# Kernel optimization log

Measured on AMD Instinct MI355X. Metric: run time of the kernel, lower is better.

Reference implementation:

```python
import jax, jax.numpy as jnp
from jax import lax
import numpy as np

B = 32768
N_IN = 8
N_HID = 64
N_CTRL = 2
M_SCEN = (1.0, 1.2)          # scenario parameters for f/g
M_NOM = 1.0
CLF_LAM = 1.0
CBF_LAM = 1.0
P_CLF = 100.0
P_CBF = 50.0
QP_ITERS = 80                # fixed-iteration batched ADMM (OSQP-style) replacing CvxpyLayer
RHO = 1.0
SIGMA = 1e-6
INF = jnp.inf


def setup_inputs() -> dict:
    key = jax.random.key(0)
    ks = jax.random.split(key, 16)
    s = 0.3
    return {
        "x":   jax.random.normal(ks[0], (B, N_IN), jnp.float32),
        "VW1": jax.random.normal(ks[1], (N_HID, N_IN), jnp.float32) * s,
        "Vb1": jax.random.normal(ks[2], (N_HID,), jnp.float32) * s,
        "VW2": jax.random.normal(ks[3], (N_HID, N_HID), jnp.float32) * s,
        "Vb2": jax.random.normal(ks[4], (N_HID,), jnp.float32) * s,
        "HW1": jax.random.normal(ks[5], (N_HID, N_IN), jnp.float32) * s,
        "Hb1": jax.random.normal(ks[6], (N_HID,), jnp.float32) * s,
        "HW2": jax.random.normal(ks[7], (N_HID, N_HID), jnp.float32) * s,
        "Hb2": jax.random.normal(ks[8], (N_HID,), jnp.float32) * s,
        "HW3": jax.random.normal(ks[9], (N_HID, N_HID), jnp.float32) * s,
        "Hb3": jax.random.normal(ks[10], (N_HID,), jnp.float32) * s,
        "HW4": jax.random.normal(ks[11], (1, N_HID), jnp.float32) * s,
        "Hb4": jax.random.normal(ks[12], (1,), jnp.float32) * s,
        "G0":  jax.random.normal(ks[13], (N_IN, N_CTRL), jnp.float32) * s,
        "K":   jax.random.normal(ks[14], (N_IN, N_CTRL), jnp.float32) * s,
    }


def _lyapunov(x, W1, b1, W2, b2):
    t1 = jnp.tanh(x @ W1.T + b1)                                   # [B,H]
    t2 = jnp.tanh(t1 @ W2.T + b2)                                  # [B,H]
    V = 0.5 * jnp.sum(t2 * t2, axis=1)                             # [B]
    # fused diag(1-t^2) @ W chain (no diag_embed materialization)
    D1 = (1.0 - t1 ** 2)[:, :, None] * W1[None]                    # [B,H,N]
    D2 = (1.0 - t2 ** 2)[:, :, None] * jnp.einsum('hk,bkn->bhn', W2, D1)
    grad_V = jnp.einsum('bh,bhn->bn', t2, D2)                      # [B,N]
    return V, grad_V


def _barrier(x, W1, b1, W2, b2, W3, b3, W4, b4):
    t1 = jnp.tanh(x @ W1.T + b1)
    t2 = jnp.tanh(t1 @ W2.T + b2)
    t3 = jnp.tanh(t2 @ W3.T + b3)
    H = t3 @ W4.T + b4                                             # [B,1]
    D1 = (1.0 - t1 ** 2)[:, :, None] * W1[None]
    D2 = (1.0 - t2 ** 2)[:, :, None] * jnp.einsum('hk,bkn->bhn', W2, D1)
    D3 = (1.0 - t3 ** 2)[:, :, None] * jnp.einsum('hk,bkn->bhn', W3, D2)
    grad_H = jnp.einsum('oh,bhn->bn', W4, D3)                      # [B,N] (o=1)
    return H, grad_H


def _solve_qp(q, A, lo, hi):
    """Batched OSQP-style ADMM for min 0.5 z^T P z + q^T z  s.t. lo <= A z <= hi.
    P = diag([2,2,0,0,0,0]); z = [u(2), r_clf(2), s_cbf(2)]. Fixed iterations."""
    nb, mc, nz = A.shape[0], A.shape[1], A.shape[2]
    Pdiag = jnp.array([2.0, 2.0, 0.0, 0.0, 0.0, 0.0], q.dtype)
    M = RHO * jnp.einsum('bmi,bmj->bij', A, A) + jnp.diag(Pdiag + SIGMA)
    Minv = jnp.linalg.inv(M)                                       # [B,6,6]
    x0 = jnp.zeros((nb, nz), q.dtype)
    z0 = jnp.zeros((nb, mc), q.dtype)
    y0 = jnp.zeros((nb, mc), q.dtype)

    def step(carry, _):
        xx, zz, yy = carry
        rhs = SIGMA * xx - q + jnp.einsum('bmi,bm->bi', A, RHO * zz - yy)
        xt = jnp.einsum('bij,bj->bi', Minv, rhs)
        zt = jnp.einsum('bmi,bi->bm', A, xt)
        zn = jnp.clip(zt + yy / RHO, lo, hi)
        yn = yy + RHO * (zt - zn)
        return (xt, zn, yn), None

    (xf, _, _), _ = lax.scan(step, (x0, z0, y0), None, length=QP_ITERS)
    return xf                                                      # [B,6]


def _forward(x, VW1, Vb1, VW2, Vb2, HW1, Hb1, HW2, Hb2, HW3, Hb3, HW4, Hb4, G0, K):
    V, grad_V = _lyapunov(x, VW1, Vb1, VW2, Vb2)
    H, grad_H = _barrier(x, HW1, Hb1, HW2, Hb2, HW3, Hb3, HW4, Hb4)

    LfVs, LgVs, LfHs, LgHs = [], [], [], []
    for m in M_SCEN:
        # f(x,m) = -x/m ; g(x,m) = G0/m
        LfVs.append(-jnp.sum(grad_V * x, axis=1) / m)              # [B]
        LgVs.append((grad_V @ G0) / m)                             # [B,C]
        LfHs.append(-jnp.sum(grad_H * x, axis=1) / m)
        LgHs.append((grad_H @ G0) / m)
    u_nom = -(x @ K) * (1.0 / M_NOM)                               # [B,C]

    nb = x.shape[0]
    z2 = jnp.zeros((nb, 2), x.dtype)
    ey = jnp.eye(2, dtype=x.dtype)
    e = lambda i: jnp.broadcast_to(ey[i], (nb, 2))
    ninf = jnp.full((nb,), -INF, x.dtype)
    pinf = jnp.full((nb,), INF, x.dtype)
    zer = jnp.zeros((nb,), x.dtype)

    rows, los, his = [], [], []
    for i in range(len(M_SCEN)):
        # CBF: LfH + LgH@u + cbf_lam*H + s_i >= 0
        rows.append(jnp.concatenate([LgHs[i], z2, e(i)], axis=1))
        los.append(-(LfHs[i] + CBF_LAM * H[:, 0])); his.append(pinf)
        # CLF: LfV + LgV@u + clf_lam*V - r_i <= 0
        rows.append(jnp.concatenate([LgVs[i], -e(i), z2], axis=1))
        los.append(ninf); his.append(-(LfVs[i] + CLF_LAM * V))
    for i in range(len(M_SCEN)):
        rows.append(jnp.concatenate([z2, e(i), z2], axis=1)); los.append(zer); his.append(pinf)
    for i in range(len(M_SCEN)):
        rows.append(jnp.concatenate([z2, z2, e(i)], axis=1)); los.append(zer); his.append(pinf)

    A = jnp.stack(rows, axis=1)                                    # [B,8,6]
    lo = jnp.stack(los, axis=1)                                    # [B,8]
    hi = jnp.stack(his, axis=1)
    # objective ||u-u_nom||^2 + p_clf*sum r + p_cbf*sum s  ->  q = [-2 u_nom, p_clf, p_clf, p_cbf, p_cbf]
    q = jnp.concatenate([-2.0 * u_nom,
                         jnp.full((nb, 2), P_CLF, x.dtype),
                         jnp.full((nb, 2), P_CBF, x.dtype)], axis=1)

    z = _solve_qp(q, A, lo, hi)                                    # [B,6]
    u = z[:, :N_CTRL]
    relaxation = jnp.mean(z[:, N_CTRL:N_CTRL + len(M_SCEN)], axis=1, keepdims=True)  # [B,1]

    ns = float(len(M_SCEN))
    Vdot = sum(LfVs[i] + jnp.sum(LgVs[i] * u, axis=1) for i in range(len(M_SCEN))) / ns
    Hdot = sum(LfHs[i] + jnp.sum(LgHs[i] * u, axis=1) for i in range(len(M_SCEN))) / ns
    return u, relaxation, V, Vdot[:, None, None], H, Hdot[:, None, None]


def reference(x, VW1, Vb1, VW2, Vb2, HW1, Hb1, HW2, Hb2, HW3, Hb3, HW4, Hb4, G0, K):
    return _forward(x, VW1, Vb1, VW2, Vb2, HW1, Hb1, HW2, Hb2, HW3, Hb3, HW4, Hb4, G0, K)
```

## Files before the change

### kernel.cpp

```cpp
#include <hip/hip_runtime.h>
#include <hip/hip_bf16.h>
#include <math.h>

typedef _Float16 f16x8 __attribute__((ext_vector_type(8)));
typedef _Float16 f16x4 __attribute__((ext_vector_type(4)));
typedef float    f32x4 __attribute__((ext_vector_type(4)));
typedef float    f32x2 __attribute__((ext_vector_type(2)));

__device__ __forceinline__ float ldin(const void* p, int i, int f32f) {
  return f32f ? ((const float*)p)[i]
              : __bfloat162float(((const __hip_bfloat16*)p)[i]);
}

__device__ __forceinline__ f32x4 MFMA(f16x8 a, f16x8 b, f32x4 c) {
  return __builtin_amdgcn_mfma_f32_16x16x32_f16(a, b, c, 0, 0, 0);
}

__device__ __forceinline__ float tanh_fast(float x) {
  float e = __expf(2.f * x);
  return 1.f - 2.f * __builtin_amdgcn_rcpf(e + 1.f);
}

__device__ __forceinline__ float redq(float v) {
  v += __shfl_xor(v, 16, 64);
  v += __shfl_xor(v, 32, 64);
  return v;
}

#define OFF_VW2   0
#define OFF_VW2T  4096
#define OFF_HW2   8192
#define OFF_HW2T  12288
#define OFF_HW3   16384
#define OFF_HW3T  20480
#define OFF_W1V   24576
#define OFF_W1H   26624
#define W_N       28672
#define CF_BASE   28672
#define C_WGV0 0
#define C_WGV1 64
#define C_WGH0 128
#define C_WGH1 192
#define C_VB1  256
#define C_VB2  320
#define C_HB1  384
#define C_HB2  448
#define C_HB3  512
#define C_W4   576
#define C_K    640
#define C_HB4  656
#define C_FLAG 657
#define C_N    658

__global__ __launch_bounds__(256) void prep_kernel(
    const void* px, const void* pVW1, const void* pVW2,
    const void* pHW1, const void* pHW2, const void* pHW3,
    const void* pVb1, const void* pVb2, const void* pHb1, const void* pHb2,
    const void* pHb3, const void* pHW4, const void* pHb4,
    const void* pG0, const void* pK, _Float16* wsp)
{
  __shared__ int sCnt;
  const int tid = threadIdx.x;
  if (tid == 0) sCnt = 0;
  __syncthreads();
  {
    const unsigned short* xb = (const unsigned short*)px;
    int good = 0;
#pragma unroll
    for (int i = 0; i < 2; ++i) {
      int ex = (xb[tid * 2 + i] >> 7) & 0xFF;
      good += (ex >= 97 && ex <= 157) ? 1 : 0;
    }
    atomicAdd(&sCnt, good);
  }
  __syncthreads();
  const int f32f = (sCnt >= 435) ? 0 : 1;

  auto ld8 = [&](const void* src, int i0, float* o) {
    if (f32f) {
      f32x4 a = *(const f32x4*)((const float*)src + i0);
      f32x4 b = *(const f32x4*)((const float*)src + i0 + 4);
#pragma unroll
      for (int j = 0; j < 4; ++j) { o[j] = a[j]; o[4 + j] = b[j]; }
    } else {
      uint4 u = *(const uint4*)((const unsigned short*)src + i0);
      unsigned uu[4] = {u.x, u.y, u.z, u.w};
#pragma unroll
      for (int j = 0; j < 4; ++j) {
        o[2 * j]     = __uint_as_float(uu[j] << 16);
        o[2 * j + 1] = __uint_as_float(uu[j] & 0xffff0000u);
      }
    }
  };

  const int bid = blockIdx.x;
  if (bid < 14) {
    const int t = bid * 256 + tid;
    if (t < 3072) {
      const int p = t >> 9, s8 = t & 511;
      const int ps = p >> 1;
      const void* src = (ps == 0) ? pVW2 : ((ps == 1) ? pHW2 : pHW3);
      const int h  = ((s8 >> 7) << 4) | (s8 & 15);
      const int k0 = (((s8 >> 6) & 1) << 5) | (((s8 >> 4) & 3) << 3);
      f16x8 v;
      if (p & 1) {
#pragma unroll
        for (int j = 0; j < 8; ++j)
          v[j] = (_Float16)ldin(src, (k0 + j) * 64 + h, f32f);
      } else {
        float o[8];
        ld8(src, h * 64 + k0, o);
#pragma unroll
        for (int j = 0; j < 8; ++j) v[j] = (_Float16)o[j];
      }
      *(f16x8*)(wsp + p * 4096 + s8 * 8) = v;
    } else {
      const int t2 = t - 3072;
      const void* src = (t2 >> 8) ? pHW1 : pVW1;
      const int off = (t2 >> 8) ? OFF_W1H : OFF_W1V;
      const int s8 = t2 & 255;
      const int mm = s8 & 15, qq = (s8 >> 4) & 3, ht = s8 >> 6;
      const int hr = ht * 16 + mm;
      float o[8];
      ld8(src, hr * 8, o);
      f16x8 v;
#pragma unroll
      for (int j = 0; j < 8; ++j) {
        _Float16 hi = (_Float16)o[j];
        v[j] = (qq < 2) ? hi
             : ((qq == 2 && f32f) ? (_Float16)(o[j] - (float)hi) : (_Float16)0.f);
      }
      *(f16x8*)(wsp + off + s8 * 8) = v;
    }
  } else {
    float* wsF = (float*)(wsp + CF_BASE);
    if (tid < 64) {
      float a0 = 0.f, a1 = 0.f, b0 = 0.f, b1 = 0.f;
#pragma unroll
      for (int nn = 0; nn < 8; ++nn) {
        float g0 = ldin(pG0, 2 * nn, f32f), g1 = ldin(pG0, 2 * nn + 1, f32f);
        float wv = ldin(pVW1, tid * 8 + nn, f32f), wh = ldin(pHW1, tid * 8 + nn, f32f);
        a0 += wv * g0; a1 += wv * g1; b0 += wh * g0; b1 += wh * g1;
      }
      wsF[C_WGV0 + tid] = a0; wsF[C_WGV1 + tid] = a1;
      wsF[C_WGH0 + tid] = b0; wsF[C_WGH1 + tid] = b1;
      wsF[C_VB1 + tid] = ldin(pVb1, tid, f32f);
      wsF[C_VB2 + tid] = ldin(pVb2, tid, f32f);
      wsF[C_HB1 + tid] = ldin(pHb1, tid, f32f);
      wsF[C_HB2 + tid] = ldin(pHb2, tid, f32f);
      wsF[C_HB3 + tid] = ldin(pHb3, tid, f32f);
      wsF[C_W4  + tid] = ldin(pHW4, tid, f32f);
    }
    if (tid < 16) wsF[C_K + tid] = ldin(pK, tid, f32f);
    if (tid == 0) { wsF[C_HB4] = ldin(pHb4, 0, f32f); ((int*)wsF)[C_FLAG] = f32f; }
  }
}

__global__ __launch_bounds__(512, 1) void main_kernel(
    const void* px, const _Float16* wsp, float* out)
{
  __shared__ __align__(16) _Float16 sW[W_N];
  __shared__ __align__(16) _Float16 sAct[16][1024];
  __shared__ __align__(16) float sQPs[10][128];
  __shared__ __align__(16) float sC[C_N];

  const int tid = threadIdx.x, lane = tid & 63, w = tid >> 6;
  const int n = lane & 15, q = lane >> 4;
  const int e0 = blockIdx.x * 128 + w * 16;

  {
    const f16x8* srcv = (const f16x8*)wsp;
    f16x8* dstv = (f16x8*)sW;
#pragma unroll
    for (int rr = 0; rr < 7; ++rr) dstv[rr * 512 + tid] = srcv[rr * 512 + tid];
  }
  const float* cf = (const float*)(wsp + CF_BASE);
  for (int i = tid; i < C_N; i += 512) sC[i] = cf[i];
  const int f32f = ((const int*)cf)[C_FLAG];

  float xv[8];
  if (f32f) {
    const f32x4* xp = (const f32x4*)((const float*)px + (e0 + n) * 8);
    f32x4 x0 = xp[0], x1 = xp[1];
#pragma unroll
    for (int j = 0; j < 4; ++j) { xv[j] = x0[j]; xv[4 + j] = x1[j]; }
  } else {
    uint4 u = *(const uint4*)((const unsigned short*)px + (e0 + n) * 8);
    unsigned uu[4] = {u.x, u.y, u.z, u.w};
#pragma unroll
    for (int j = 0; j < 4; ++j) {
      xv[2 * j]     = __uint_as_float(uu[j] << 16);
      xv[2 * j + 1] = __uint_as_float(uu[j] & 0xffff0000u);
    }
  }
  __syncthreads();

  float un0 = 0.f, un1 = 0.f;
  f16x8 xb;
#pragma unroll
  for (int j = 0; j < 8; ++j) {
    _Float16 hh = (_Float16)xv[j];
    float lo = xv[j] - (float)hh;
    xb[j] = (q == 1) ? (_Float16)lo : ((q == 3) ? (_Float16)0.f : hh);
    un0 -= xv[j] * sC[C_K + 2 * j];
    un1 -= xv[j] * sC[C_K + 2 * j + 1];
  }

  _Float16* bufV = sAct[2 * w];
  _Float16* bufH = sAct[2 * w + 1];

  auto gemm64x2 = [&](int poffV, int poffH, f32x4* accV, f32x4* accH) {
    f16x8 aV[8], aH[8];
#pragma unroll
    for (int i = 0; i < 8; ++i)
      aV[i] = *(const f16x8*)(sW + poffV + i * 512 + lane * 8);
#pragma unroll
    for (int i = 0; i < 8; ++i)
      aH[i] = *(const f16x8*)(sW + poffH + i * 512 + lane * 8);
    f16x8 bV0 = *(const f16x8*)(bufV + lane * 8);
    f16x8 bV1 = *(const f16x8*)(bufV + 512 + lane * 8);
    f16x8 bH0 = *(const f16x8*)(bufH + lane * 8);
    f16x8 bH1 = *(const f16x8*)(bufH + 512 + lane * 8);
#pragma unroll
    for (int ht = 0; ht < 4; ++ht) {
      f32x4 c = {0.f, 0.f, 0.f, 0.f};
      c = MFMA(aV[2 * ht], bV0, c);
      accV[ht] = MFMA(aV[2 * ht + 1], bV1, c);
      f32x4 d = {0.f, 0.f, 0.f, 0.f};
      d = MFMA(aH[2 * ht], bH0, d);
      accH[ht] = MFMA(aH[2 * ht + 1], bH1, d);
    }
  };
  auto gemm64 = [&](int poff, const _Float16* b, f32x4* acc) {
    f16x8 a[8];
#pragma unroll
    for (int i = 0; i < 8; ++i)
      a[i] = *(const f16x8*)(sW + poff + i * 512 + lane * 8);
    f16x8 b0 = *(const f16x8*)(b + lane * 8);
    f16x8 b1 = *(const f16x8*)(b + 512 + lane * 8);
#pragma unroll
    for (int ht = 0; ht < 4; ++ht) {
      f32x4 c = {0.f, 0.f, 0.f, 0.f};
      c = MFMA(a[2 * ht], b0, c);
      acc[ht] = MFMA(a[2 * ht + 1], b1, c);
    }
  };
  auto l1gemm2 = [&](f32x4* accV, f32x4* accH) {
    f16x8 aV[4], aH[4];
#pragma unroll
    for (int ht = 0; ht < 4; ++ht)
      aV[ht] = *(const f16x8*)(sW + OFF_W1V + ht * 512 + lane * 8);
#pragma unroll
    for (int ht = 0; ht < 4; ++ht)
      aH[ht] = *(const f16x8*)(sW + OFF_W1H + ht * 512 + lane * 8);
#pragma unroll
    for (int ht = 0; ht < 4; ++ht) {
      f32x4 c = {0.f, 0.f, 0.f, 0.f};
      accV[ht] = MFMA(aV[ht], xb, c);
      f32x4 d = {0.f, 0.f, 0.f, 0.f};
      accH[ht] = MFMA(aH[ht], xb, d);
    }
  };
  auto wst = [&](const f32x4* vals, _Float16* b) {
#pragma unroll
    for (int ht = 0; ht < 4; ++ht) {
      int aw = ((ht >> 1) << 9) + (((ht & 1) * 2 + (q >> 1)) << 7) + n * 8 + ((q & 1) << 2);
      f16x4 vh;
#pragma unroll
      for (int r = 0; r < 4; ++r) vh[r] = (_Float16)vals[ht][r];
      *(f16x4*)(b + aw) = vh;
    }
  };

  f32x4 accV[4], accH[4], tvV[4], tvH[4];
  f32x4 z1V[4], d1V[4], z1H[4], d1H[4], d2H[4];

  l1gemm2(accV, accH);
#pragma unroll
  for (int ht = 0; ht < 4; ++ht) {
    int hb = ht * 16 + q * 4;
    f32x4 bV = *(const f32x4*)&sC[C_VB1 + hb];
    f32x4 bH = *(const f32x4*)&sC[C_HB1 + hb];
    z1V[ht] = accV[ht]; z1H[ht] = accH[ht];
#pragma unroll
    for (int r = 0; r < 4; ++r) {
      float t = tanh_fast(z1V[ht][r] + bV[r]);
      tvV[ht][r] = t; d1V[ht][r] = 1.f - t * t;
      t = tanh_fast(z1H[ht][r] + bH[r]);
      tvH[ht][r] = t; d1H[ht][r] = 1.f - t * t;
    }
  }
  wst(tvV, bufV); wst(tvH, bufH);

  gemm64x2(OFF_VW2, OFF_HW2, accV, accH);
  float pV = 0.f;
#pragma unroll
  for (int ht = 0; ht < 4; ++ht) {
    int hb = ht * 16 + q * 4;
    f32x4 bV = *(const f32x4*)&sC[C_VB2 + hb];
    f32x4 bH = *(const f32x4*)&sC[C_HB2 + hb];
#pragma unroll
    for (int r = 0; r < 4; ++r) {
      float t = tanh_fast(accV[ht][r] + bV[r]);
      pV += t * t;
      tvV[ht][r] = t * (1.f - t * t);
      t = tanh_fast(accH[ht][r] + bH[r]);
      tvH[ht][r] = t; d2H[ht][r] = 1.f - t * t;
    }
  }
  wst(tvV, bufV); wst(tvH, bufH);

  gemm64x2(OFF_VW2T, OFF_HW3, accV, accH);
  float pgvx = 0.f, plv0 = 0.f, plv1 = 0.f, pH = 0.f;
#pragma unroll
  for (int ht = 0; ht < 4; ++ht) {
    int hb = ht * 16 + q * 4;
    f32x4 g0 = *(const f32x4*)&sC[C_WGV0 + hb];
    f32x4 g1 = *(const f32x4*)&sC[C_WGV1 + hb];
    f32x4 bH = *(const f32x4*)&sC[C_HB3 + hb];
    f32x4 w4 = *(const f32x4*)&sC[C_W4 + hb];
#pragma unroll
    for (int r = 0; r < 4; ++r) {
      float wt = accV[ht][r] * d1V[ht][r];
      pgvx += wt * z1V[ht][r];
      plv0 += wt * g0[r]; plv1 += wt * g1[r];
      float t = tanh_fast(accH[ht][r] + bH[r]);
      pH += t * w4[r];
      tvH[ht][r] = w4[r] * (1.f - t * t);
    }
  }
  wst(tvH, bufH);

  gemm64(OFF_HW3T, bufH, accH);
#pragma unroll
  for (int ht = 0; ht < 4; ++ht)
#pragma unroll
    for (int r = 0; r < 4; ++r) tvH[ht][r] = accH[ht][r] * d2H[ht][r];
  wst(tvH, bufH);

  gemm64(OFF_HW2T, bufH, accH);
  float pghx = 0.f, plh0 = 0.f, plh1 = 0.f;
#pragma unroll
  for (int ht = 0; ht < 4; ++ht) {
    int hb = ht * 16 + q * 4;
    f32x4 g0 = *(const f32x4*)&sC[C_WGH0 + hb];
    f32x4 g1 = *(const f32x4*)&sC[C_WGH1 + hb];
#pragma unroll
    for (int r = 0; r < 4; ++r) {
      float wt = accH[ht][r] * d1H[ht][r];
      pghx += wt * z1H[ht][r];
      plh0 += wt * g0[r]; plh1 += wt * g1[r];
    }
  }

  {
    float a0 = redq(plh0), a1 = redq(plh1), a2 = redq(plv0), a3 = redq(plv1);
    float a4 = redq(pghx), a5 = redq(pgvx), a6 = redq(pV), a7 = redq(pH);
    if (q == 0) {
      int col = w * 16 + n;
      sQPs[0][col] = a0; sQPs[1][col] = a1; sQPs[2][col] = a2; sQPs[3][col] = a3;
      sQPs[4][col] = a4; sQPs[5][col] = a5; sQPs[6][col] = a6; sQPs[7][col] = a7;
      sQPs[8][col] = un0; sQPs[9][col] = un1;
    }
  }
  __syncthreads();
  if (w != 0 && w != 2) return;

  const int col = (w >> 1) * 64 + lane;
  const int e = blockIdx.x * 128 + col;
  float gh0 = sQPs[0][col], gh1 = sQPs[1][col];
  float gv0 = sQPs[2][col], gv1 = sQPs[3][col];
  float ghx = sQPs[4][col], gvx = sQPs[5][col];
  float V   = 0.5f * sQPs[6][col];
  float H   = sQPs[7][col] + sC[C_HB4];
  un0 = sQPs[8][col]; un1 = sQPs[9][col];
  out[98304 + e]  = V;
  out[163840 + e] = H;

  const float im = 1.0f / 1.2f;
  const float sg = 1e-6f;
  const float d  = 2.f + sg;
  const float rd = 1.f / d;
  const float al = 1.f + im * im;
  const float be = al * (1.f - rd);
  float S00 = be * (gh0 * gh0 + gv0 * gv0) + d;
  float S11 = be * (gh1 * gh1 + gv1 * gv1) + d;
  float S01 = be * (gh0 * gh1 + gv0 * gv1);
  float idet = 1.f / (S00 * S11 - S01 * S01);

  f32x2 IM2; IM2[0] = 1.f; IM2[1] = im;
  f32x2 ghP; ghP[0] = gh0; ghP[1] = gh1;
  f32x2 gvP; gvP[0] = gv0; gvP[1] = gv1;
  f32x2 gHV0; gHV0[0] = gh0; gHV0[1] = gv0;
  f32x2 gHV1; gHV1[0] = gh1; gHV1[1] = gv1;
  f32x2 iA; iA[0] = S11 * idet;  iA[1] = -S01 * idet;
  f32x2 iB; iB[0] = -S01 * idet; iB[1] = S00 * idet;
  f32x2 nqP; nqP[0] = 2.f * un0; nqP[1] = 2.f * un1;
  f32x2 loA; loA[0] = ghx - H;      loA[1] = ghx * im - H;
  f32x2 hiB; hiB[0] = gvx - V;      hiB[1] = gvx * im - V;

  f32x2 ZA = {0.f, 0.f}, ZB = {0.f, 0.f}, ZC = {0.f, 0.f}, ZD = {0.f, 0.f};
  f32x2 YA = {0.f, 0.f}, YB = {0.f, 0.f}, YC = {0.f, 0.f}, YD = {0.f, 0.f};
  f32x2 X01 = {0.f, 0.f}, XP = {0.f, 0.f}, XS = {0.f, 0.f};

#pragma unroll 1
  for (int it = 0; it < 80; ++it) {
    f32x2 tA = ZA - YA, tB = ZB - YB, tC = ZC - YC, tD = ZD - YD;
    float tauh = tA[0] + im * tA[1];
    float tauv = tB[0] + im * tB[1];
    f32x2 bU = nqP + ghP * tauh + gvP * tauv;
    f32x2 bP = tC - tB - 100.f;
    f32x2 bS = tA + tD - 50.f;
    float pp = bP[0] + im * bP[1];
    float s2 = bS[0] + im * bS[1];
    f32x2 cb = ghP * s2 - gvP * pp;
    f32x2 ub = bU - cb * rd;
    X01 = iA * ub[0] + iB * ub[1];
    f32x2 gd = gHV0 * X01[0] + gHV1 * X01[1];
    XP = (bP + IM2 * gd[1]) * rd;
    XS = (bS - IM2 * gd[0]) * rd;
    f32x2 ztA = IM2 * gd[0] + XS;
    f32x2 ztB = IM2 * gd[1] - XP;

    f32x2 vv, zn;
    vv = ztA + YA; zn[0] = fmaxf(vv[0], loA[0]); zn[1] = fmaxf(vv[1], loA[1]);
    YA += ztA - zn; ZA = zn;
    vv = ztB + YB; zn[0] = fminf(vv[0], hiB[0]); zn[1] = fminf(vv[1], hiB[1]);
    YB += ztB - zn; ZB = zn;
    vv = XP + YC;  zn[0] = fmaxf(vv[0], 0.f);   zn[1] = fmaxf(vv[1], 0.f);
    YC += XP - zn; ZC = zn;
    vv = XS + YD;  zn[0] = fmaxf(vv[0], 0.f);   zn[1] = fmaxf(vv[1], 0.f);
    YD += XS - zn; ZD = zn;
  }

  float relax = 0.5f * (XP[0] + XP[1]);
  const float cc = 0.5f * (1.f + im);
  float Vdot = cc * (gv0 * X01[0] + gv1 * X01[1] - gvx);
  float Hdot = cc * (gh0 * X01[0] + gh1 * X01[1] - ghx);

  f32x2 uo; uo[0] = X01[0]; uo[1] = X01[1];
  *(f32x2*)&out[2 * e] = uo;
  out[65536 + e]  = relax;
  out[131072 + e] = Vdot;
  out[196608 + e] = Hdot;
}

extern "C" void kernel_launch(void* const* d_in, const int* in_sizes, int n_in,
                              void* d_out, int out_size, void* d_ws, size_t ws_size,
                              hipStream_t stream) {
  (void)in_sizes; (void)n_in; (void)out_size; (void)ws_size;
  float* out = (float*)d_out;
  _Float16* wsp = (_Float16*)d_ws;
  prep_kernel<<<15, 256, 0, stream>>>(
      d_in[0], d_in[1], d_in[3], d_in[5], d_in[7], d_in[9],
      d_in[2], d_in[4], d_in[6], d_in[8], d_in[10], d_in[11], d_in[12],
      d_in[13], d_in[14], wsp);
  main_kernel<<<256, 512, 0, stream>>>(d_in[0], wsp, out);
}
```

Measured before the change: 103.8 us.

## Fuse weight-prep kernel into main kernel, building shared weights per block

Removes the separate prep kernel and its workspace round-trip. Each block now converts the raw weights into the fp16 MFMA layout and computes the constant table directly in shared memory. This saves a kernel launch and the dependency between the two kernels. The cost is redundant weight conversion in all 256 blocks, including strided transposed global reads. It also changes the dtype-detection threshold for the larger sample and simplifies the ADMM dual update to reuse the computed sum.

```diff
diff --git a/kernel.cpp b/kernel.cpp
--- a/kernel.cpp
+++ b/kernel.cpp
@@ -36,7 +36,6 @@
 #define OFF_W1V   24576
 #define OFF_W1H   26624
 #define W_N       28672
-#define CF_BASE   28672
 #define C_WGV0 0
 #define C_WGV1 64
 #define C_WGH0 128
@@ -49,32 +48,54 @@
 #define C_W4   576
 #define C_K    640
 #define C_HB4  656
-#define C_FLAG 657
 #define C_N    658
 
-__global__ __launch_bounds__(256) void prep_kernel(
-    const void* px, const void* pVW1, const void* pVW2,
-    const void* pHW1, const void* pHW2, const void* pHW3,
-    const void* pVb1, const void* pVb2, const void* pHb1, const void* pHb2,
-    const void* pHb3, const void* pHW4, const void* pHb4,
-    const void* pG0, const void* pK, _Float16* wsp)
+__global__ __launch_bounds__(512, 1) void fused_kernel(
+    const void* px, const void* pVW1, const void* pVb1, const void* pVW2, const void* pVb2,
+    const void* pHW1, const void* pHb1, const void* pHW2, const void* pHb2,
+    const void* pHW3, const void* pHb3, const void* pHW4, const void* pHb4,
+    const void* pG0, const void* pK, float* out)
 {
+  __shared__ __align__(16) _Float16 sW[W_N];
+  __shared__ __align__(16) _Float16 sAct[16][1024];
+  __shared__ __align__(16) float sQPs[10][128];
+  __shared__ __align__(16) float sC[C_N];
   __shared__ int sCnt;
-  const int tid = threadIdx.x;
+
+  const int tid = threadIdx.x, lane = tid & 63, w = tid >> 6;
+  const int n = lane & 15, q = lane >> 4;
+  const int e0 = blockIdx.x * 128 + w * 16;
+
   if (tid == 0) sCnt = 0;
   __syncthreads();
   {
-    const unsigned short* xb = (const unsigned short*)px;
+    const unsigned short* xbp = (const unsigned short*)px;
     int good = 0;
 #pragma unroll
     for (int i = 0; i < 2; ++i) {
-      int ex = (xb[tid * 2 + i] >> 7) & 0xFF;
+      int ex = (xbp[tid * 2 + i] >> 7) & 0xFF;
       good += (ex >= 97 && ex <= 157) ? 1 : 0;
     }
     atomicAdd(&sCnt, good);
   }
   __syncthreads();
-  const int f32f = (sCnt >= 435) ? 0 : 1;
+  const int f32f = (sCnt >= 870) ? 0 : 1;
+
+  float xv[8];
+  if (f32f) {
+    const f32x4* xp = (const f32x4*)((const float*)px + (e0 + n) * 8);
+    f32x4 x0 = xp[0], x1 = xp[1];
+#pragma unroll
+    for (int j = 0; j < 4; ++j) { xv[j] = x0[j]; xv[4 + j] = x1[j]; }
+  } else {
+    uint4 u = *(const uint4*)((const unsigned short*)px + (e0 + n) * 8);
+    unsigned uu[4] = {u.x, u.y, u.z, u.w};
+#pragma unroll
+    for (int j = 0; j < 4; ++j) {
+      xv[2 * j]     = __uint_as_float(uu[j] << 16);
+      xv[2 * j + 1] = __uint_as_float(uu[j] & 0xffff0000u);
+    }
+  }
 
   auto ld8 = [&](const void* src, int i0, float* o) {
     if (f32f) {
@@ -93,15 +114,13 @@
     }
   };
 
-  const int bid = blockIdx.x;
-  if (bid < 14) {
-    const int t = bid * 256 + tid;
-    if (t < 3072) {
-      const int p = t >> 9, s8 = t & 511;
-      const int ps = p >> 1;
-      const void* src = (ps == 0) ? pVW2 : ((ps == 1) ? pHW2 : pHW3);
-      const int h  = ((s8 >> 7) << 4) | (s8 & 15);
-      const int k0 = (((s8 >> 6) & 1) << 5) | (((s8 >> 4) & 3) << 3);
+  {
+    const int s8 = tid & 511;
+    const int h  = ((s8 >> 7) << 4) | (s8 & 15);
+    const int k0 = (((s8 >> 6) & 1) << 5) | (((s8 >> 4) & 3) << 3);
+#pragma unroll
+    for (int p = 0; p < 6; ++p) {
+      const void* src = (p < 2) ? pVW2 : ((p < 4) ? pHW2 : pHW3);
       f16x8 v;
       if (p & 1) {
 #pragma unroll
@@ -113,16 +132,16 @@
 #pragma unroll
         for (int j = 0; j < 8; ++j) v[j] = (_Float16)o[j];
       }
-      *(f16x8*)(wsp + p * 4096 + s8 * 8) = v;
-    } else {
-      const int t2 = t - 3072;
+      *(f16x8*)(sW + p * 4096 + s8 * 8) = v;
+    }
+    {
+      const int t2 = tid;
       const void* src = (t2 >> 8) ? pHW1 : pVW1;
       const int off = (t2 >> 8) ? OFF_W1H : OFF_W1V;
-      const int s8 = t2 & 255;
-      const int mm = s8 & 15, qq = (s8 >> 4) & 3, ht = s8 >> 6;
-      const int hr = ht * 16 + mm;
+      const int ss = t2 & 255;
+      const int mm = ss & 15, qq = (ss >> 4) & 3, ht = ss >> 6;
       float o[8];
-      ld8(src, hr * 8, o);
+      ld8(src, (ht * 16 + mm) * 8, o);
       f16x8 v;
 #pragma unroll
       for (int j = 0; j < 8; ++j) {
@@ -130,69 +149,30 @@
         v[j] = (qq < 2) ? hi
              : ((qq == 2 && f32f) ? (_Float16)(o[j] - (float)hi) : (_Float16)0.f);
       }
-      *(f16x8*)(wsp + off + s8 * 8) = v;
-    }
-  } else {
-    float* wsF = (float*)(wsp + CF_BASE);
-    if (tid < 64) {
-      float a0 = 0.f, a1 = 0.f, b0 = 0.f, b1 = 0.f;
-#pragma unroll
-      for (int nn = 0; nn < 8; ++nn) {
-        float g0 = ldin(pG0, 2 * nn, f32f), g1 = ldin(pG0, 2 * nn + 1, f32f);
-        float wv = ldin(pVW1, tid * 8 + nn, f32f), wh = ldin(pHW1, tid * 8 + nn, f32f);
-        a0 += wv * g0; a1 += wv * g1; b0 += wh * g0; b1 += wh * g1;
-      }
-      wsF[C_WGV0 + tid] = a0; wsF[C_WGV1 + tid] = a1;
-      wsF[C_WGH0 + tid] = b0; wsF[C_WGH1 + tid] = b1;
-      wsF[C_VB1 + tid] = ldin(pVb1, tid, f32f);
-      wsF[C_VB2 + tid] = ldin(pVb2, tid, f32f);
-      wsF[C_HB1 + tid] = ldin(pHb1, tid, f32f);
-      wsF[C_HB2 + tid] = ldin(pHb2, tid, f32f);
-      wsF[C_HB3 + tid] = ldin(pHb3, tid, f32f);
-      wsF[C_W4  + tid] = ldin(pHW4, tid, f32f);
-    }
-    if (tid < 16) wsF[C_K + tid] = ldin(pK, tid, f32f);
-    if (tid == 0) { wsF[C_HB4] = ldin(pHb4, 0, f32f); ((int*)wsF)[C_FLAG] = f32f; }
-  }
-}
-
-__global__ __launch_bounds__(512, 1) void main_kernel(
-    const void* px, const _Float16* wsp, float* out)
-{
-  __shared__ __align__(16) _Float16 sW[W_N];
-  __shared__ __align__(16) _Float16 sAct[16][1024];
-  __shared__ __align__(16) float sQPs[10][128];
-  __shared__ __align__(16) float sC[C_N];
-
-  const int tid = threadIdx.x, lane = tid & 63, w = tid >> 6;
-  const int n = lane & 15, q = lane >> 4;
-  const int e0 = blockIdx.x * 128 + w * 16;
-
-  {
-    const f16x8* srcv = (const f16x8*)wsp;
-    f16x8* dstv = (f16x8*)sW;
-#pragma unroll
-    for (int rr = 0; rr < 7; ++rr) dstv[rr * 512 + tid] = srcv[rr * 512 + tid];
-  }
-  const float* cf = (const float*)(wsp + CF_BASE);
-  for (int i = tid; i < C_N; i += 512) sC[i] = cf[i];
-  const int f32f = ((const int*)cf)[C_FLAG];
-
-  float xv[8];
-  if (f32f) {
-    const f32x4* xp = (const f32x4*)((const float*)px + (e0 + n) * 8);
-    f32x4 x0 = xp[0], x1 = xp[1];
-#pragma unroll
-    for (int j = 0; j < 4; ++j) { xv[j] = x0[j]; xv[4 + j] = x1[j]; }
-  } else {
-    uint4 u = *(const uint4*)((const unsigned short*)px + (e0 + n) * 8);
-    unsigned uu[4] = {u.x, u.y, u.z, u.w};
-#pragma unroll
-    for (int j = 0; j < 4; ++j) {
-      xv[2 * j]     = __uint_as_float(uu[j] << 16);
-      xv[2 * j + 1] = __uint_as_float(uu[j] & 0xffff0000u);
-    }
-  }
+      *(f16x8*)(sW + off + ss * 8) = v;
+    }
+  }
+
+  if (tid < 64) {
+    float a0 = 0.f, a1 = 0.f, b0 = 0.f, b1 = 0.f;
+#pragma unroll
+    for (int nn = 0; nn < 8; ++nn) {
+      float g0 = ldin(pG0, 2 * nn, f32f), g1 = ldin(pG0, 2 * nn + 1, f32f);
+      float wv = ldin(pVW1, tid * 8 + nn, f32f), wh = ldin(pHW1, tid * 8 + nn, f32f);
+      a0 += wv * g0; a1 += wv * g1; b0 += wh * g0; b1 += wh * g1;
+    }
+    sC[C_WGV0 + tid] = a0; sC[C_WGV1 + tid] = a1;
+    sC[C_WGH0 + tid] = b0; sC[C_WGH1 + tid] = b1;
+    sC[C_VB1 + tid] = ldin(pVb1, tid, f32f);
+    sC[C_VB2 + tid] = ldin(pVb2, tid, f32f);
+    sC[C_HB1 + tid] = ldin(pHb1, tid, f32f);
+    sC[C_HB2 + tid] = ldin(pHb2, tid, f32f);
+    sC[C_HB3 + tid] = ldin(pHb3, tid, f32f);
+    sC[C_W4  + tid] = ldin(pHW4, tid, f32f);
+  }
+  if (tid < 16) sC[C_K + tid] = ldin(pK, tid, f32f);
+  if (tid == 0) sC[C_HB4] = ldin(pHb4, 0, f32f);
+
   __syncthreads();
 
   float un0 = 0.f, un1 = 0.f;
@@ -424,13 +404,13 @@
 
     f32x2 vv, zn;
     vv = ztA + YA; zn[0] = fmaxf(vv[0], loA[0]); zn[1] = fmaxf(vv[1], loA[1]);
-    YA += ztA - zn; ZA = zn;
+    YA = vv - zn; ZA = zn;
     vv = ztB + YB; zn[0] = fminf(vv[0], hiB[0]); zn[1] = fminf(vv[1], hiB[1]);
-    YB += ztB - zn; ZB = zn;
+    YB = vv - zn; ZB = zn;
     vv = XP + YC;  zn[0] = fmaxf(vv[0], 0.f);   zn[1] = fmaxf(vv[1], 0.f);
-    YC += XP - zn; ZC = zn;
+    YC = vv - zn; ZC = zn;
     vv = XS + YD;  zn[0] = fmaxf(vv[0], 0.f);   zn[1] = fmaxf(vv[1], 0.f);
-    YD += XS - zn; ZD = zn;
+    YD = vv - zn; ZD = zn;
   }
 
   float relax = 0.5f * (XP[0] + XP[1]);
@@ -448,12 +428,9 @@
 extern "C" void kernel_launch(void* const* d_in, const int* in_sizes, int n_in,
                               void* d_out, int out_size, void* d_ws, size_t ws_size,
                               hipStream_t stream) {
-  (void)in_sizes; (void)n_in; (void)out_size; (void)ws_size;
-  float* out = (float*)d_out;
-  _Float16* wsp = (_Float16*)d_ws;
-  prep_kernel<<<15, 256, 0, stream>>>(
-      d_in[0], d_in[1], d_in[3], d_in[5], d_in[7], d_in[9],
-      d_in[2], d_in[4], d_in[6], d_in[8], d_in[10], d_in[11], d_in[12],
-      d_in[13], d_in[14], wsp);
-  main_kernel<<<256, 512, 0, stream>>>(d_in[0], wsp, out);
-}
+  (void)in_sizes; (void)n_in; (void)out_size; (void)d_ws; (void)ws_size;
+  fused_kernel<<<256, 512, 0, stream>>>(
+      d_in[0], d_in[1], d_in[2], d_in[3], d_in[4], d_in[5], d_in[6],
+      d_in[7], d_in[8], d_in[9], d_in[10], d_in[11], d_in[12],
+      d_in[13], d_in[14], (float*)d_out);
+}
```

New measurement: 101.4 us. 2.3% less time.
